# Optimization experiments

Measured on AMD Instinct MI355X. Metric: run time of the kernel, lower is better.

The kernel has to match this reference:

```python
import jax, jax.numpy as jnp
import numpy as np

T, B, IN, OUT, N_MOD, K = 1024, 8, 1024, 1024, 16, 2

def setup_inputs() -> dict:
    key = jax.random.key(0)
    k1, k2, k3, k4 = jax.random.split(key, 4)
    x = jax.random.normal(k1, (T, B, IN), dtype=jnp.float32)
    selection = jax.random.randint(k2, (B, K), 0, N_MOD, dtype=jnp.int64)
    weight = jax.random.normal(k3, (N_MOD, IN, OUT), dtype=jnp.float32) * (1.0 / np.sqrt(IN))
    bias = jax.random.normal(k4, (N_MOD, OUT), dtype=jnp.float32) * 0.02
    return {"x": x, "selection": selection, "weight": weight, "bias": bias}

def reference(x, selection, weight, bias):
    # time_major=True: x is [T, B, in] -> batch-major [B, T, in]
    xb = jnp.swapaxes(x, 0, 1)
    # Gather the K selected expert weight matrices per batch row: [B, K, in, out]
    W_sel = weight[selection]
    # Equivalent to matmul(x[i], cat(weight[sel], dim=1)): [B, T, K, out]
    o = jnp.einsum('bti,bkio->btko', xb, W_sel)
    Bn, Tn, Kn, On = o.shape
    o = o.reshape(Bn, Tn, Kn * On)
    # concat_dim == 1 bias: bias[sel].view(1, -1) -> [1, K*out], broadcast over T
    o = o + bias[selection].reshape(Bn, 1, Kn * On)
    # back to time-major [T, B, K*out]
    return jnp.swapaxes(o, 0, 1)
```

## Files before the change

kernel.cpp:

```cpp
#include <hip/hip_runtime.h>

#define T_DIM 1024
#define B_DIM 8
#define IN_DIM 1024
#define OUT_DIM 1024
#define N_MODL 16
#define K_SEL 2

typedef unsigned short ushort_t;
typedef __bf16 bf16x8 __attribute__((ext_vector_type(8)));
typedef float f32x4 __attribute__((ext_vector_type(4)));

__device__ __forceinline__ unsigned short f2bf(float f) {
  union { float f; unsigned int u; } v; v.f = f;
  unsigned int r = v.u + 0x7fffu + ((v.u >> 16) & 1u);
  return (unsigned short)(r >> 16);
}

__device__ __forceinline__ void async_g2l(const void* g, void* l) {
  __builtin_amdgcn_global_load_lds(
      (const __attribute__((address_space(1))) unsigned int*)g,
      (__attribute__((address_space(3))) unsigned int*)l,
      16, 0, 0);
}

__global__ __launch_bounds__(256) void convert_x_kernel(const float* __restrict__ x,
                                                        ushort_t* __restrict__ xb) {
  const int row = blockIdx.x;
  const int t = row >> 3, b = row & 7;
  const float4* src = (const float4*)(x + (size_t)row * IN_DIM);
  ushort_t* dst = xb + ((size_t)b * T_DIM + t) * IN_DIM;
  float4 v = src[threadIdx.x];
  ushort4 o;
  o.x = f2bf(v.x); o.y = f2bf(v.y); o.z = f2bf(v.z); o.w = f2bf(v.w);
  *(ushort4*)(dst + threadIdx.x * 4) = o;
}

__global__ __launch_bounds__(256) void convert_w_kernel(const float* __restrict__ w,
                                                        ushort_t* __restrict__ wt) {
  __shared__ float tile[64][65];
  const int m = blockIdx.z;
  const int i0 = blockIdx.x * 64;
  const int o0 = blockIdx.y * 64;
  const float* src = w + ((size_t)m * IN_DIM + i0) * OUT_DIM + o0;
  const int c = (threadIdx.x & 15) * 4;
  const int r0 = threadIdx.x >> 4;
#pragma unroll
  for (int p = 0; p < 4; ++p) {
    const int r = r0 + p * 16;
    float4 v = *(const float4*)(src + (size_t)r * OUT_DIM + c);
    tile[r][c + 0] = v.x; tile[r][c + 1] = v.y;
    tile[r][c + 2] = v.z; tile[r][c + 3] = v.w;
  }
  __syncthreads();
  ushort_t* dst = wt + ((size_t)m * OUT_DIM + o0) * IN_DIM + i0;
#pragma unroll
  for (int p = 0; p < 4; ++p) {
    const int r = r0 + p * 16;
    ushort4 ov;
    ov.x = f2bf(tile[c + 0][r]);
    ov.y = f2bf(tile[c + 1][r]);
    ov.z = f2bf(tile[c + 2][r]);
    ov.w = f2bf(tile[c + 3][r]);
    *(ushort4*)(dst + (size_t)r * IN_DIM + c) = ov;
  }
}

__device__ __forceinline__ int read_sel(const int* __restrict__ s, int g) {
  bool i64 = true;
#pragma unroll
  for (int j = 0; j < 8; ++j) i64 &= (s[2 * j + 1] == 0);
  return i64 ? s[2 * g] : s[g];
}

__global__ __launch_bounds__(256) void mlgemm_kernel(const ushort_t* __restrict__ xb,
                                                     const ushort_t* __restrict__ wt,
                                                     const int* __restrict__ selp,
                                                     const float* __restrict__ bias,
                                                     float* __restrict__ out) {
  __shared__ ushort_t As[128 * 64];
  __shared__ ushort_t Bs[128 * 64];

  const int g = blockIdx.z;
  const int b = g >> 1, ks = g & 1;
  const int e = read_sel(selp, g);

  const ushort_t* A  = xb + (size_t)b * T_DIM * IN_DIM;
  const ushort_t* Bm = wt + (size_t)e * OUT_DIM * IN_DIM;
  const float* bp = bias + (size_t)e * OUT_DIM;

  const int m0 = blockIdx.y * 128;
  const int n0 = blockIdx.x * 128;

  const int tid = threadIdx.x;
  const int lane = tid & 63;
  const int wv = tid >> 6;

  const int srow = lane >> 3;
  const int scol = (lane & 7) * 8;
  const ushort_t* Abase = A  + (size_t)(m0 + srow) * IN_DIM + scol;
  const ushort_t* Bbase = Bm + (size_t)(n0 + srow) * IN_DIM + scol;

  const int frow = lane & 15;
  const int fk = (lane >> 4) * 8;
  const int wrow = (wv & 1) * 64;
  const int wcol = (wv >> 1) * 64;
  const ushort_t* Ard = As + (wrow + frow) * 64 + fk;
  const ushort_t* Brd = Bs + (wcol + frow) * 64 + fk;

  f32x4 acc[4][4] = {};

  for (int k0 = 0; k0 < IN_DIM; k0 += 64) {
#pragma unroll
    for (int c = 0; c < 4; ++c) {
      const int chunk = wv * 4 + c;
      async_g2l(Abase + (size_t)chunk * 8 * IN_DIM + k0, As + chunk * 512);
      async_g2l(Bbase + (size_t)chunk * 8 * IN_DIM + k0, Bs + chunk * 512);
    }
    __syncthreads();
#pragma unroll
    for (int kk = 0; kk < 64; kk += 32) {
      bf16x8 af[4], bfr[4];
#pragma unroll
      for (int i = 0; i < 4; ++i) {
        af[i]  = *(const bf16x8*)(Ard + i * 16 * 64 + kk);
        bfr[i] = *(const bf16x8*)(Brd + i * 16 * 64 + kk);
      }
#pragma unroll
      for (int mt = 0; mt < 4; ++mt)
#pragma unroll
        for (int nt = 0; nt < 4; ++nt)
          acc[mt][nt] = __builtin_amdgcn_mfma_f32_16x16x32_bf16(af[mt], bfr[nt],
                                                                acc[mt][nt], 0, 0, 0);
    }
    __syncthreads();
  }

  const int orow0 = m0 + wrow + ((lane >> 4) * 4);
  const int ocol0 = n0 + wcol + (lane & 15);
  float bv[4];
#pragma unroll
  for (int nt = 0; nt < 4; ++nt) bv[nt] = bp[ocol0 + nt * 16];
  float* Cb = out + (size_t)b * (K_SEL * OUT_DIM) + (size_t)ks * OUT_DIM;
#pragma unroll
  for (int mt = 0; mt < 4; ++mt) {
#pragma unroll
    for (int r = 0; r < 4; ++r) {
      const size_t rowoff = (size_t)(orow0 + mt * 16 + r) * (B_DIM * K_SEL * OUT_DIM);
#pragma unroll
      for (int nt = 0; nt < 4; ++nt)
        Cb[rowoff + ocol0 + nt * 16] = acc[mt][nt][r] + bv[nt];
    }
  }
}

extern "C" void kernel_launch(void* const* d_in, const int* in_sizes, int n_in,
                              void* d_out, int out_size, void* d_ws, size_t ws_size,
                              hipStream_t stream) {
  const float* x    = (const float*)d_in[0];
  const int*   sel  = (const int*)d_in[1];
  const float* w    = (const float*)d_in[2];
  const float* bias = (const float*)d_in[3];
  float* out = (float*)d_out;

  ushort_t* xb = (ushort_t*)d_ws;
  ushort_t* wt = (ushort_t*)((char*)d_ws +
                             (size_t)B_DIM * T_DIM * IN_DIM * 2);

  convert_x_kernel<<<dim3(T_DIM * B_DIM), 256, 0, stream>>>(x, xb);
  convert_w_kernel<<<dim3(IN_DIM / 64, OUT_DIM / 64, N_MODL), 256, 0, stream>>>(w, wt);
  mlgemm_kernel<<<dim3(OUT_DIM / 128, T_DIM / 128, B_DIM * K_SEL), 256, 0, stream>>>(
      xb, wt, sel, bias, out);
}
```

Before: 203.2 us.

## Swizzle LDS tiles, keep x time-major in bf16, add occupancy hint

Converts x to bf16 in its original time-major layout with a flat, wider-vector conversion kernel that writes packed pairs, and makes the GEMM read A rows with a stride of B*IN. LDS tiles for A and B now use an XOR swizzle on 16-byte chunks, applied both when the async global-to-LDS loads are issued and when fragments are read, to avoid bank conflicts. The GEMM also gets a launch_bounds minimum of 4 blocks per SM. The strided A rows may reduce global-load locality, and the occupancy hint may limit register allocation.

Measured after the change: 186.9 us. 8.0% less time.

```diff
diff --git a/kernel.cpp b/kernel.cpp
--- a/kernel.cpp
+++ b/kernel.cpp
@@ -11,10 +11,15 @@
 typedef __bf16 bf16x8 __attribute__((ext_vector_type(8)));
 typedef float f32x4 __attribute__((ext_vector_type(4)));
 
+__device__ __forceinline__ unsigned int f2bf2(float lo, float hi) {
+  union { float f; unsigned int u; } a, b; a.f = lo; b.f = hi;
+  unsigned int ra = (a.u + 0x7fffu + ((a.u >> 16) & 1u)) >> 16;
+  unsigned int rb = (b.u + 0x7fffu + ((b.u >> 16) & 1u)) >> 16;
+  return ra | (rb << 16);
+}
 __device__ __forceinline__ unsigned short f2bf(float f) {
   union { float f; unsigned int u; } v; v.f = f;
-  unsigned int r = v.u + 0x7fffu + ((v.u >> 16) & 1u);
-  return (unsigned short)(r >> 16);
+  return (unsigned short)((v.u + 0x7fffu + ((v.u >> 16) & 1u)) >> 16);
 }
 
 __device__ __forceinline__ void async_g2l(const void* g, void* l) {
@@ -26,14 +31,13 @@
 
 __global__ __launch_bounds__(256) void convert_x_kernel(const float* __restrict__ x,
                                                         ushort_t* __restrict__ xb) {
-  const int row = blockIdx.x;
-  const int t = row >> 3, b = row & 7;
-  const float4* src = (const float4*)(x + (size_t)row * IN_DIM);
-  ushort_t* dst = xb + ((size_t)b * T_DIM + t) * IN_DIM;
-  float4 v = src[threadIdx.x];
-  ushort4 o;
-  o.x = f2bf(v.x); o.y = f2bf(v.y); o.z = f2bf(v.z); o.w = f2bf(v.w);
-  *(ushort4*)(dst + threadIdx.x * 4) = o;
+  const int i = blockIdx.x * 256 + threadIdx.x;
+  const float4* s = (const float4*)x;
+  float4 a = s[i * 2], b = s[i * 2 + 1];
+  uint4 o;
+  o.x = f2bf2(a.x, a.y); o.y = f2bf2(a.z, a.w);
+  o.z = f2bf2(b.x, b.y); o.w = f2bf2(b.z, b.w);
+  ((uint4*)xb)[i] = o;
 }
 
 __global__ __launch_bounds__(256) void convert_w_kernel(const float* __restrict__ w,
@@ -73,11 +77,11 @@
   return i64 ? s[2 * g] : s[g];
 }
 
-__global__ __launch_bounds__(256) void mlgemm_kernel(const ushort_t* __restrict__ xb,
-                                                     const ushort_t* __restrict__ wt,
-                                                     const int* __restrict__ selp,
-                                                     const float* __restrict__ bias,
-                                                     float* __restrict__ out) {
+__global__ __launch_bounds__(256, 4) void mlgemm_kernel(const ushort_t* __restrict__ xb,
+                                                        const ushort_t* __restrict__ wt,
+                                                        const int* __restrict__ selp,
+                                                        const float* __restrict__ bias,
+                                                        float* __restrict__ out) {
   __shared__ ushort_t As[128 * 64];
   __shared__ ushort_t Bs[128 * 64];
 
@@ -85,7 +89,7 @@
   const int b = g >> 1, ks = g & 1;
   const int e = read_sel(selp, g);
 
-  const ushort_t* A  = xb + (size_t)b * T_DIM * IN_DIM;
+  const ushort_t* A  = xb + (size_t)b * IN_DIM;
   const ushort_t* Bm = wt + (size_t)e * OUT_DIM * IN_DIM;
   const float* bp = bias + (size_t)e * OUT_DIM;
 
@@ -97,34 +101,36 @@
   const int wv = tid >> 6;
 
   const int srow = lane >> 3;
-  const int scol = (lane & 7) * 8;
-  const ushort_t* Abase = A  + (size_t)(m0 + srow) * IN_DIM + scol;
-  const ushort_t* Bbase = Bm + (size_t)(n0 + srow) * IN_DIM + scol;
+  const int sx = (((lane & 7) ^ (srow & 7)) << 3);
+  const ushort_t* Ab = A  + (size_t)(m0 + srow) * (B_DIM * IN_DIM) + sx;
+  const ushort_t* Bb = Bm + (size_t)(n0 + srow) * IN_DIM + sx;
 
   const int frow = lane & 15;
-  const int fk = (lane >> 4) * 8;
+  const int quad = lane >> 4;
+  const int cbase = ((quad ^ (frow & 7)) << 3);
   const int wrow = (wv & 1) * 64;
   const int wcol = (wv >> 1) * 64;
-  const ushort_t* Ard = As + (wrow + frow) * 64 + fk;
-  const ushort_t* Brd = Bs + (wcol + frow) * 64 + fk;
+  const ushort_t* Ard = As + (wrow + frow) * 64;
+  const ushort_t* Brd = Bs + (wcol + frow) * 64;
 
   f32x4 acc[4][4] = {};
 
   for (int k0 = 0; k0 < IN_DIM; k0 += 64) {
 #pragma unroll
     for (int c = 0; c < 4; ++c) {
-      const int chunk = wv * 4 + c;
-      async_g2l(Abase + (size_t)chunk * 8 * IN_DIM + k0, As + chunk * 512);
-      async_g2l(Bbase + (size_t)chunk * 8 * IN_DIM + k0, Bs + chunk * 512);
+      const int j = wv * 4 + c;
+      async_g2l(Ab + (size_t)(8 * j) * (B_DIM * IN_DIM) + k0, As + j * 512);
+      async_g2l(Bb + (size_t)(8 * j) * IN_DIM + k0, Bs + j * 512);
     }
     __syncthreads();
 #pragma unroll
     for (int kk = 0; kk < 64; kk += 32) {
+      const int coff = cbase ^ kk;
       bf16x8 af[4], bfr[4];
 #pragma unroll
       for (int i = 0; i < 4; ++i) {
-        af[i]  = *(const bf16x8*)(Ard + i * 16 * 64 + kk);
-        bfr[i] = *(const bf16x8*)(Brd + i * 16 * 64 + kk);
+        af[i]  = *(const bf16x8*)(Ard + i * 16 * 64 + coff);
+        bfr[i] = *(const bf16x8*)(Brd + i * 16 * 64 + coff);
       }
 #pragma unroll
       for (int mt = 0; mt < 4; ++mt)
@@ -136,8 +142,8 @@
     __syncthreads();
   }
 
-  const int orow0 = m0 + wrow + ((lane >> 4) * 4);
-  const int ocol0 = n0 + wcol + (lane & 15);
+  const int orow0 = m0 + wrow + (quad * 4);
+  const int ocol0 = n0 + wcol + frow;
   float bv[4];
 #pragma unroll
   for (int nt = 0; nt < 4; ++nt) bv[nt] = bp[ocol0 + nt * 16];
@@ -165,9 +171,9 @@
 
   ushort_t* xb = (ushort_t*)d_ws;
   ushort_t* wt = (ushort_t*)((char*)d_ws +
-                             (size_t)B_DIM * T_DIM * IN_DIM * 2);
+                             (size_t)T_DIM * B_DIM * IN_DIM * 2);
 
-  convert_x_kernel<<<dim3(T_DIM * B_DIM), 256, 0, stream>>>(x, xb);
+  convert_x_kernel<<<dim3(T_DIM * B_DIM * IN_DIM / 8 / 256), 256, 0, stream>>>(x, xb);
   convert_w_kernel<<<dim3(IN_DIM / 64, OUT_DIM / 64, N_MODL), 256, 0, stream>>>(w, wt);
   mlgemm_kernel<<<dim3(OUT_DIM / 128, T_DIM / 128, B_DIM * K_SEL), 256, 0, stream>>>(
       xb, wt, sel, bias, out);
```
